# Optimization experiments

Measured on AMD Instinct MI355X. Metric: run time of the kernel, lower is better.

## Reference

```python
import jax, jax.numpy as jnp
import numpy as np
from jax.scipy.special import logsumexp

D = 256; H = 8; A = D // H
B_CONST = 0.9; P_MAX = 50000.0; P_MIN = 1e-4; TANH_RATE = 0.005; EPS = 1e-10
SCALE = 1.0 / np.sqrt(D)


def setup_inputs() -> dict:
    key = jax.random.key(0)
    ks = jax.random.split(key, 5)
    B, S = 2, 512
    context = jax.random.normal(ks[0], (B, S, D), dtype=jnp.float32)
    W_Q = jax.random.normal(ks[1], (D, D), dtype=jnp.float32) * (1.0 / np.sqrt(D))
    W_KV = jax.random.normal(ks[2], (2 * D, D), dtype=jnp.float32) * (1.0 / np.sqrt(D))
    W_out = jax.random.normal(ks[3], (D, D), dtype=jnp.float32) * (1.0 / np.sqrt(D))
    p_param = jax.random.normal(ks[4], (D,), dtype=jnp.float32) * 0.02
    return {"context": context, "W_Q": W_Q, "W_KV": W_KV, "W_out": W_out, "p_param": p_param}


def reference(context, W_Q, W_KV, W_out, p_param):
    B, S, _ = context.shape
    # projections (nn.Linear: x @ W.T)
    q = context @ W_Q.T                          # [B,S,D]
    kv = context @ W_KV.T                        # [B,S,2D]
    k, v = kv[..., :D], kv[..., D:]
    # scaled p: p_max*tanh(tanh_rate*p)+1, then replace exact zeros with p_min
    p = P_MAX * jnp.tanh(TANH_RATE * p_param) + 1.0
    p = p + (p == 0).astype(p.dtype) * P_MIN
    # minmax-normalize v over the key/sequence axis into [b, 1]
    v_max = jnp.max(v, axis=-2, keepdims=True)   # [B,1,D]
    v_min = jnp.min(v, axis=-2, keepdims=True)
    v = (1.0 - B_CONST) * (v - v_min) / (v_max - v_min + EPS) + B_CONST
    z = p * jnp.log(v)                           # [B,S,D]
    # split heads
    qh = q.reshape(B, S, H, A).transpose(0, 2, 1, 3)          # [B,H,S,A]
    kh = k.reshape(B, S, H, A).transpose(0, 2, 1, 3)          # [B,H,S,A]
    zh = z.reshape(B, S, H, A).transpose(0, 2, 1, 3)[:, :, None]  # [B,H,1,K,A]
    dot = jnp.einsum('bhqa,bhka->bhqk', qh, kh)
    w = jax.nn.log_softmax(dot * SCALE, axis=-1)              # [B,H,Q,K]
    # log-domain power mean: logsumexp over keys of log-weights + p*log(v)
    mean = logsumexp(w[..., None] + zh, axis=-2)              # [B,H,Q,A]
    mean = mean.transpose(0, 2, 1, 3).reshape(B, S, D)
    e = jnp.exp(mean / p)
    # invert v minmax normalization
    e = (e - B_CONST) * (v_max - v_min + EPS) / (1.0 - B_CONST) + v_min
    return e @ W_out.T
```

## Files before the change

kernel.cpp:

```cpp
#include <hip/hip_runtime.h>
#include <math.h>

#define DD 256
#define HH 8
#define AA 32
#define SS 512
#define BB 2
constexpr float BCONST      = 0.9f;
constexpr float ONE_MINUS_B = 0.1f;
constexpr float EPSF        = 1e-10f;
constexpr float SCALEF      = 0.0625f;
constexpr float FLTMAX      = 3.402823466e38f;

#define OFF_QKV    0
#define OFF_VP     786432
#define OFF_EW     1048576
#define OFF_PMIN   1310720
#define OFF_PMAX   1318912
#define OFF_VMIN   1327104
#define OFF_VRANGE 1327616
#define OFF_P      1328128

#define KB4(buf, row, col4) \
  (&(buf)[((row) << 5) | ((((col4) >> 2) ^ (((row) >> 2) & 7)) << 2)])

template<int TM, int TN, int RM, int RN, bool MM>
__global__ __launch_bounds__(256) void gemm_t(
    const float* __restrict__ A, const float* __restrict__ B0,
    const float* __restrict__ B1, int nsplit,
    float* __restrict__ C, int ldc, int K, int lda,
    float* __restrict__ pminP, float* __restrict__ pmaxP) {
  constexpr int LDT = 36;
  constexpr int CG  = TN / RN;
  constexpr int NA  = TM * 32 / 1024;
  constexpr int NB  = TN * 32 / 1024;
  __shared__ float As[TM][LDT];
  __shared__ float Bs[TN][LDT];
  const int i0 = blockIdx.x * TM;
  const int j0 = blockIdx.y * TN;
  const float* Bsrc = (j0 < nsplit) ? (B0 + (size_t)j0 * K)
                                    : (B1 + (size_t)(j0 - nsplit) * K);
  const int t  = threadIdx.x;
  const int lr = t >> 3;
  const int lc = (t & 7) << 2;
  const int tx = t % CG, ty = t / CG;

  float4 pa[NA], pb[NB];
#pragma unroll
  for (int u = 0; u < NA; ++u)
    pa[u] = *(const float4*)(A + (size_t)(i0 + lr + 32 * u) * lda + lc);
#pragma unroll
  for (int u = 0; u < NB; ++u)
    pb[u] = *(const float4*)(Bsrc + (size_t)(lr + 32 * u) * K + lc);

  float acc[RM][RN] = {};
  for (int k0 = 0; k0 < K; k0 += 32) {
    __syncthreads();
#pragma unroll
    for (int u = 0; u < NA; ++u) *(float4*)&As[lr + 32 * u][lc] = pa[u];
#pragma unroll
    for (int u = 0; u < NB; ++u) *(float4*)&Bs[lr + 32 * u][lc] = pb[u];
    __syncthreads();
    if (k0 + 32 < K) {
#pragma unroll
      for (int u = 0; u < NA; ++u)
        pa[u] = *(const float4*)(A + (size_t)(i0 + lr + 32 * u) * lda + k0 + 32 + lc);
#pragma unroll
      for (int u = 0; u < NB; ++u)
        pb[u] = *(const float4*)(Bsrc + (size_t)(lr + 32 * u) * K + k0 + 32 + lc);
    }
#pragma unroll
    for (int kk = 0; kk < 32; kk += 4) {
      float4 af[RM], bf[RN];
#pragma unroll
      for (int r = 0; r < RM; ++r) af[r] = *(const float4*)&As[ty * RM + r][kk];
#pragma unroll
      for (int c = 0; c < RN; ++c) bf[c] = *(const float4*)&Bs[tx + CG * c][kk];
#pragma unroll
      for (int r = 0; r < RM; ++r)
#pragma unroll
        for (int c = 0; c < RN; ++c)
          acc[r][c] += af[r].x * bf[c].x + af[r].y * bf[c].y +
                       af[r].z * bf[c].z + af[r].w * bf[c].w;
    }
  }
#pragma unroll
  for (int r = 0; r < RM; ++r)
#pragma unroll
    for (int c = 0; c < RN; ++c)
      C[(size_t)(i0 + ty * RM + r) * ldc + j0 + tx + CG * c] = acc[r][c];

  if (MM && j0 >= 512) {
    __syncthreads();
    float* mnb = &As[0][0];
    float* mxb = &Bs[0][0];
#pragma unroll
    for (int c = 0; c < RN; ++c) {
      float mn = acc[0][c], mx = acc[0][c];
#pragma unroll
      for (int r = 1; r < RM; ++r) {
        mn = fminf(mn, acc[r][c]);
        mx = fmaxf(mx, acc[r][c]);
      }
      mnb[(tx + CG * c) * 17 + ty] = mn;
      mxb[(tx + CG * c) * 17 + ty] = mx;
    }
    __syncthreads();
    if (t < TN) {
      float mn = mnb[t * 17], mx = mxb[t * 17];
#pragma unroll
      for (int i = 1; i < 16; ++i) {
        mn = fminf(mn, mnb[t * 17 + i]);
        mx = fmaxf(mx, mxb[t * 17 + i]);
      }
      const int bx = i0 >> 5;
      pminP[bx * 256 + (j0 - 512) + t] = mn;
      pmaxP[bx * 256 + (j0 - 512) + t] = mx;
    }
  }
}

__global__ __launch_bounds__(256) void vpk(
    const float* __restrict__ qkv, const float* __restrict__ pminP,
    const float* __restrict__ pmaxP, const float* __restrict__ p_param,
    float* __restrict__ vp, float* __restrict__ vminw,
    float* __restrict__ vrangew, float* __restrict__ pw) {
  const int blk = blockIdx.x;
  const int b = blk >> 9, s = blk & 511;
  const int d = threadIdx.x;
  float mn = pminP[(b * 16) * 256 + d];
  float mx = pmaxP[(b * 16) * 256 + d];
#pragma unroll
  for (int c = 1; c < 16; ++c) {
    mn = fminf(mn, pminP[(b * 16 + c) * 256 + d]);
    mx = fmaxf(mx, pmaxP[(b * 16 + c) * 256 + d]);
  }
  float p = 50000.0f * tanhf(0.005f * p_param[d]) + 1.0f;
  if (p == 0.0f) p = 0.0001f;
  const float range = mx - mn + EPSF;
  const float v  = qkv[((size_t)(b * 512 + s)) * 768 + 512 + d];
  const float vn = (ONE_MINUS_B * (v - mn)) / range + BCONST;
  vp[(size_t)blk * 256 + d] = expm1f(p * logf(vn));
  if (s == 0) { vminw[b * 256 + d] = mn; vrangew[b * 256 + d] = range; }
  if (blk == 0) pw[d] = p;
}

__global__ __launch_bounds__(256) void attn_k(
    const float* __restrict__ qkv, const float* __restrict__ vp,
    const float* __restrict__ pw, const float* __restrict__ vminw,
    const float* __restrict__ vrangew, float* __restrict__ ew) {
  __shared__ float qs[16][36];
  __shared__ float scT[512 * 20];
  __shared__ float kb[256 * 32];
  __shared__ float red[16][17];
  const int bh  = blockIdx.x;
  const int b   = bh >> 3, h = bh & 7;
  const int q0g = blockIdx.y * 16;
  const int t   = threadIdx.x;
  const int ldr = t >> 3, ldc4 = (t & 7) << 2;

  if (t < 128) {
    const int q = t >> 3, c4 = (t & 7) << 2;
    float4 qv = *(const float4*)(qkv + ((size_t)(b * 512 + q0g + q)) * 768 + h * 32 + c4);
    qv.x *= SCALEF; qv.y *= SCALEF; qv.z *= SCALEF; qv.w *= SCALEF;
    *(float4*)&qs[q][c4] = qv;
  }

  float4 pk[8];
#pragma unroll
  for (int u = 0; u < 8; ++u)
    pk[u] = *(const float4*)(qkv + ((size_t)(b * 512 + ldr + 32 * u)) * 768 + 256 + h * 32 + ldc4);

  const int qg = t & 3;
  const int kg = t >> 2;
  for (int kc = 0; kc < 2; ++kc) {
    __syncthreads();
#pragma unroll
    for (int u = 0; u < 8; ++u) *(float4*)KB4(kb, ldr + 32 * u, ldc4) = pk[u];
    __syncthreads();
    if (kc == 0) {
#pragma unroll
      for (int u = 0; u < 8; ++u)
        pk[u] = *(const float4*)(qkv + ((size_t)(b * 512 + 256 + ldr + 32 * u)) * 768 + 256 + h * 32 + ldc4);
    } else {
#pragma unroll
      for (int u = 0; u < 8; ++u)
        pk[u] = *(const float4*)(vp + ((size_t)(b * 512 + ldr + 32 * u)) * 256 + h * 32 + ldc4);
    }
    float a2[4][4] = {};
#pragma unroll
    for (int kk = 0; kk < 32; kk += 4) {
      float4 qf[4], kf[4];
#pragma unroll
      for (int r = 0; r < 4; ++r) qf[r] = *(const float4*)&qs[qg * 4 + r][kk];
#pragma unroll
      for (int c = 0; c < 4; ++c) kf[c] = *(const float4*)KB4(kb, kg * 4 + c, kk);
#pragma unroll
      for (int r = 0; r < 4; ++r)
#pragma unroll
        for (int c = 0; c < 4; ++c)
          a2[r][c] += qf[r].x * kf[c].x + qf[r].y * kf[c].y +
                      qf[r].z * kf[c].z + qf[r].w * kf[c].w;
    }
#pragma unroll
    for (int c = 0; c < 4; ++c)
      *(float4*)&scT[(kc * 256 + kg * 4 + c) * 20 + qg * 4] =
          make_float4(a2[0][c], a2[1][c], a2[2][c], a2[3][c]);
  }
  __syncthreads();

  {
    const int q = t & 15, j = t >> 4;
    float m = -FLTMAX;
#pragma unroll
    for (int i = 0; i < 32; ++i) m = fmaxf(m, scT[(j * 32 + i) * 20 + q]);
    red[q][j] = m;
    __syncthreads();
    float rm = red[q][0];
#pragma unroll
    for (int jj = 1; jj < 16; ++jj) rm = fmaxf(rm, red[q][jj]);
    __syncthreads();
    float ls = 0.f;
#pragma unroll
    for (int i = 0; i < 32; ++i) {
      float e = __expf(scT[(j * 32 + i) * 20 + q] - rm);
      scT[(j * 32 + i) * 20 + q] = e;
      ls += e;
    }
    red[q][j] = ls;
    __syncthreads();
    if (j == 0) {
      float tot = 0.f;
#pragma unroll
      for (int jj = 0; jj < 16; ++jj) tot += red[q][jj];
      red[q][16] = tot;
    }
  }

  float a3[4][4] = {};
  const int qg3 = t & 3;
  const int ag3 = (t >> 2) & 7;
  const int ks  = t >> 5;
  for (int kc = 0; kc < 2; ++kc) {
    __syncthreads();
#pragma unroll
    for (int u = 0; u < 8; ++u) *(float4*)KB4(kb, ldr + 32 * u, ldc4) = pk[u];
    __syncthreads();
    if (kc == 0) {
#pragma unroll
      for (int u = 0; u < 8; ++u)
        pk[u] = *(const float4*)(vp + ((size_t)(b * 512 + 256 + ldr + 32 * u)) * 256 + h * 32 + ldc4);
    }
#pragma unroll
    for (int g = 0; g < 8; ++g) {
#pragma unroll
      for (int c = 0; c < 4; ++c) {
        const int k = ks * 32 + g * 4 + c;
        const float4 sq = *(const float4*)&scT[(kc * 256 + k) * 20 + qg3 * 4];
        const float4 vf = *(const float4*)KB4(kb, k, ag3 * 4);
        a3[0][0] += sq.x * vf.x; a3[0][1] += sq.x * vf.y; a3[0][2] += sq.x * vf.z; a3[0][3] += sq.x * vf.w;
        a3[1][0] += sq.y * vf.x; a3[1][1] += sq.y * vf.y; a3[1][2] += sq.y * vf.z; a3[1][3] += sq.y * vf.w;
        a3[2][0] += sq.z * vf.x; a3[2][1] += sq.z * vf.y; a3[2][2] += sq.z * vf.z; a3[2][3] += sq.z * vf.w;
        a3[3][0] += sq.w * vf.x; a3[3][1] += sq.w * vf.y; a3[3][2] += sq.w * vf.z; a3[3][3] += sq.w * vf.w;
      }
    }
  }

#pragma unroll
  for (int r = 0; r < 4; ++r)
#pragma unroll
    for (int c = 0; c < 4; ++c)
      a3[r][c] += __shfl_xor(a3[r][c], 32);
  __syncthreads();
  float* part2 = &kb[0];
  if ((t & 32) == 0) {
    const int w = t >> 6;
#pragma unroll
    for (int r = 0; r < 4; ++r)
#pragma unroll
      for (int c = 0; c < 4; ++c)
        part2[w * 520 + (qg3 * 4 + r) * 32 + ag3 * 4 + c] = a3[r][c];
  }
  __syncthreads();
  {
    const int q = t >> 4, a = (t * 2) & 31;
    const float invT = 1.0f / red[q][16];
    float o2[2];
#pragma unroll
    for (int o = 0; o < 2; ++o) {
      const int ia = q * 32 + a + o;
      float s = part2[ia] + part2[520 + ia] + part2[1040 + ia] + part2[1560 + ia];
      s *= invT;
      const int d = h * 32 + a + o;
      const float p = pw[d];
      const float mean = log1pf(s);
      const float en = expf(mean / p);
      o2[o] = (en - BCONST) * vrangew[b * 256 + d] / ONE_MINUS_B + vminw[b * 256 + d];
    }
    *(float2*)(ew + ((size_t)(b * 512 + q0g + q)) * 256 + h * 32 + a) =
        make_float2(o2[0], o2[1]);
  }
}

extern "C" void kernel_launch(void* const* d_in, const int* in_sizes, int n_in,
                              void* d_out, int out_size, void* d_ws, size_t ws_size,
                              hipStream_t stream) {
  const float* ctx  = (const float*)d_in[0];
  const float* WQ   = (const float*)d_in[1];
  const float* WKV  = (const float*)d_in[2];
  const float* WOUT = (const float*)d_in[3];
  const float* PP   = (const float*)d_in[4];
  float* ws      = (float*)d_ws;
  float* qkv     = ws + OFF_QKV;
  float* vp      = ws + OFF_VP;
  float* ew      = ws + OFF_EW;
  float* pminP   = ws + OFF_PMIN;
  float* pmaxP   = ws + OFF_PMAX;
  float* vminw   = ws + OFF_VMIN;
  float* vrangew = ws + OFF_VRANGE;
  float* pw      = ws + OFF_P;
  float* out     = (float*)d_out;

  gemm_t<32, 64, 2, 4, true><<<dim3(32, 12), 256, 0, stream>>>(
      ctx, WQ, WKV, 256, qkv, 768, 256, 256, pminP, pmaxP);
  vpk<<<1024, 256, 0, stream>>>(qkv, pminP, pmaxP, PP, vp, vminw, vrangew, pw);
  attn_k<<<dim3(16, 32), 256, 0, stream>>>(qkv, vp, pw, vminw, vrangew, ew);
  gemm_t<32, 32, 2, 2, false><<<dim3(32, 8), 256, 0, stream>>>(
      ew, WOUT, WOUT, 1 << 30, out, 256, 256, 256, nullptr, nullptr);
}
```

Measured before the change: 124.6 us.

## Replace GEMM tiles with wave-uniform B loads and split-K atomics for output projection

```diff
diff --git a/kernel.cpp b/kernel.cpp
--- a/kernel.cpp
+++ b/kernel.cpp
@@ -24,96 +24,84 @@
 #define KB4(buf, row, col4) \
   (&(buf)[((row) << 5) | ((((col4) >> 2) ^ (((row) >> 2) & 7)) << 2)])
 
-template<int TM, int TN, int RM, int RN, bool MM>
-__global__ __launch_bounds__(256) void gemm_t(
+template<int KBT, bool MM, bool ATOM>
+__global__ __launch_bounds__(256) void gemm_s(
     const float* __restrict__ A, const float* __restrict__ B0,
     const float* __restrict__ B1, int nsplit,
-    float* __restrict__ C, int ldc, int K, int lda,
+    float* __restrict__ C, int ldc, int lda, int K,
     float* __restrict__ pminP, float* __restrict__ pmaxP) {
-  constexpr int LDT = 36;
-  constexpr int CG  = TN / RN;
-  constexpr int NA  = TM * 32 / 1024;
-  constexpr int NB  = TN * 32 / 1024;
-  __shared__ float As[TM][LDT];
-  __shared__ float Bs[TN][LDT];
-  const int i0 = blockIdx.x * TM;
-  const int j0 = blockIdx.y * TN;
-  const float* Bsrc = (j0 < nsplit) ? (B0 + (size_t)j0 * K)
-                                    : (B1 + (size_t)(j0 - nsplit) * K);
-  const int t  = threadIdx.x;
-  const int lr = t >> 3;
-  const int lc = (t & 7) << 2;
-  const int tx = t % CG, ty = t / CG;
-
-  float4 pa[NA], pb[NB];
-#pragma unroll
-  for (int u = 0; u < NA; ++u)
-    pa[u] = *(const float4*)(A + (size_t)(i0 + lr + 32 * u) * lda + lc);
-#pragma unroll
-  for (int u = 0; u < NB; ++u)
-    pb[u] = *(const float4*)(Bsrc + (size_t)(lr + 32 * u) * K + lc);
-
-  float acc[RM][RN] = {};
-  for (int k0 = 0; k0 < K; k0 += 32) {
-    __syncthreads();
-#pragma unroll
-    for (int u = 0; u < NA; ++u) *(float4*)&As[lr + 32 * u][lc] = pa[u];
-#pragma unroll
-    for (int u = 0; u < NB; ++u) *(float4*)&Bs[lr + 32 * u][lc] = pb[u];
-    __syncthreads();
-    if (k0 + 32 < K) {
-#pragma unroll
-      for (int u = 0; u < NA; ++u)
-        pa[u] = *(const float4*)(A + (size_t)(i0 + lr + 32 * u) * lda + k0 + 32 + lc);
-#pragma unroll
-      for (int u = 0; u < NB; ++u)
-        pb[u] = *(const float4*)(Bsrc + (size_t)(lr + 32 * u) * K + k0 + 32 + lc);
-    }
-#pragma unroll
-    for (int kk = 0; kk < 32; kk += 4) {
-      float4 af[RM], bf[RN];
-#pragma unroll
-      for (int r = 0; r < RM; ++r) af[r] = *(const float4*)&As[ty * RM + r][kk];
-#pragma unroll
-      for (int c = 0; c < RN; ++c) bf[c] = *(const float4*)&Bs[tx + CG * c][kk];
-#pragma unroll
-      for (int r = 0; r < RM; ++r)
-#pragma unroll
-        for (int c = 0; c < RN; ++c)
-          acc[r][c] += af[r].x * bf[c].x + af[r].y * bf[c].y +
-                       af[r].z * bf[c].z + af[r].w * bf[c].w;
-    }
-  }
-#pragma unroll
-  for (int r = 0; r < RM; ++r)
-#pragma unroll
-    for (int c = 0; c < RN; ++c)
-      C[(size_t)(i0 + ty * RM + r) * ldc + j0 + tx + CG * c] = acc[r][c];
+  constexpr int LD = KBT + 4;
+  __shared__ float A_lds[64 * LD];
+  const int i0  = blockIdx.x * 64;
+  const int j0  = blockIdx.y * 64;
+  const int kb0 = ATOM ? blockIdx.z * KBT : 0;
+  const int t   = threadIdx.x;
+  const int l   = t & 63;
+
+  constexpr int TPR = KBT / 4;
+  constexpr int RPP = 256 / TPR;
+  const int srow = t / TPR, scol = (t % TPR) * 4;
+#pragma unroll
+  for (int p = 0; p < 64 / RPP; ++p) {
+    const int r = p * RPP + srow;
+    float4 v = *(const float4*)(A + (size_t)(i0 + r) * lda + kb0 + scol);
+    *(float4*)&A_lds[r * LD + scol] = v;
+  }
+  __syncthreads();
+
+  const int w   = __builtin_amdgcn_readfirstlane(t >> 6);
+  const int j0w = j0 + w * 16;
+  const float* Bw = (j0w < nsplit)
+      ? (B0 + (size_t)j0w * (size_t)K + kb0)
+      : (B1 + (size_t)(j0w - nsplit) * (size_t)K + kb0);
+
+  float acc[16] = {};
+#pragma unroll 2
+  for (int k0 = 0; k0 < KBT; k0 += 8) {
+    const float4 a0 = *(const float4*)&A_lds[l * LD + k0];
+    const float4 a1 = *(const float4*)&A_lds[l * LD + k0 + 4];
+    const float af[8] = {a0.x, a0.y, a0.z, a0.w, a1.x, a1.y, a1.z, a1.w};
+#pragma unroll
+    for (int jg = 0; jg < 4; ++jg) {
+      const float* br = Bw + (size_t)(jg * 4) * K + k0;
+      float bv[4][8];
+#pragma unroll
+      for (int c = 0; c < 4; ++c)
+#pragma unroll
+        for (int x = 0; x < 8; ++x) bv[c][x] = br[(size_t)c * K + x];
+#pragma unroll
+      for (int c = 0; c < 4; ++c)
+#pragma unroll
+        for (int x = 0; x < 8; ++x)
+          acc[jg * 4 + c] += af[x] * bv[c][x];
+    }
+  }
+
+  const size_t crow = (size_t)(i0 + l) * ldc + j0w;
+  if (!ATOM) {
+#pragma unroll
+    for (int jg = 0; jg < 4; ++jg)
+      *(float4*)(C + crow + jg * 4) =
+          make_float4(acc[jg * 4], acc[jg * 4 + 1], acc[jg * 4 + 2], acc[jg * 4 + 3]);
+  } else {
+#pragma unroll
+    for (int u = 0; u < 16; ++u) atomicAdd(C + crow + u, acc[u]);
+  }
 
   if (MM && j0 >= 512) {
     __syncthreads();
-    float* mnb = &As[0][0];
-    float* mxb = &Bs[0][0];
-#pragma unroll
-    for (int c = 0; c < RN; ++c) {
-      float mn = acc[0][c], mx = acc[0][c];
-#pragma unroll
-      for (int r = 1; r < RM; ++r) {
-        mn = fminf(mn, acc[r][c]);
-        mx = fmaxf(mx, acc[r][c]);
+#pragma unroll
+    for (int u = 0; u < 16; ++u) A_lds[l * LD + w * 16 + u] = acc[u];
+    __syncthreads();
+    if (t < 64) {
+      float mn = A_lds[t], mx = mn;
+#pragma unroll
+      for (int r = 1; r < 64; ++r) {
+        const float v = A_lds[r * LD + t];
+        mn = fminf(mn, v);
+        mx = fmaxf(mx, v);
       }
-      mnb[(tx + CG * c) * 17 + ty] = mn;
-      mxb[(tx + CG * c) * 17 + ty] = mx;
-    }
-    __syncthreads();
-    if (t < TN) {
-      float mn = mnb[t * 17], mx = mxb[t * 17];
-#pragma unroll
-      for (int i = 1; i < 16; ++i) {
-        mn = fminf(mn, mnb[t * 17 + i]);
-        mx = fmaxf(mx, mxb[t * 17 + i]);
-      }
-      const int bx = i0 >> 5;
+      const int bx = blockIdx.x;
       pminP[bx * 256 + (j0 - 512) + t] = mn;
       pmaxP[bx * 256 + (j0 - 512) + t] = mx;
     }
@@ -128,12 +116,12 @@
   const int blk = blockIdx.x;
   const int b = blk >> 9, s = blk & 511;
   const int d = threadIdx.x;
-  float mn = pminP[(b * 16) * 256 + d];
-  float mx = pmaxP[(b * 16) * 256 + d];
-#pragma unroll
-  for (int c = 1; c < 16; ++c) {
-    mn = fminf(mn, pminP[(b * 16 + c) * 256 + d]);
-    mx = fmaxf(mx, pmaxP[(b * 16 + c) * 256 + d]);
+  float mn = pminP[(b * 8) * 256 + d];
+  float mx = pmaxP[(b * 8) * 256 + d];
+#pragma unroll
+  for (int c = 1; c < 8; ++c) {
+    mn = fminf(mn, pminP[(b * 8 + c) * 256 + d]);
+    mx = fmaxf(mx, pmaxP[(b * 8 + c) * 256 + d]);
   }
   float p = 50000.0f * tanhf(0.005f * p_param[d]) + 1.0f;
   if (p == 0.0f) p = 0.0001f;
@@ -321,10 +309,11 @@
   float* pw      = ws + OFF_P;
   float* out     = (float*)d_out;
 
-  gemm_t<32, 64, 2, 4, true><<<dim3(32, 12), 256, 0, stream>>>(
+  gemm_s<256, true, false><<<dim3(16, 12), 256, 0, stream>>>(
       ctx, WQ, WKV, 256, qkv, 768, 256, 256, pminP, pmaxP);
   vpk<<<1024, 256, 0, stream>>>(qkv, pminP, pmaxP, PP, vp, vminw, vrangew, pw);
   attn_k<<<dim3(16, 32), 256, 0, stream>>>(qkv, vp, pw, vminw, vrangew, ew);
-  gemm_t<32, 32, 2, 2, false><<<dim3(32, 8), 256, 0, stream>>>(
+  hipMemsetAsync(out, 0, (size_t)out_size * sizeof(float), stream);
+  gemm_s<64, false, true><<<dim3(16, 4, 4), 256, 0, stream>>>(
       ew, WOUT, WOUT, 1 << 30, out, 256, 256, 256, nullptr, nullptr);
 }
```

Measured after the change: 216.8 us. 74.1% more time.
